# Kernel optimization log

Measured on AMD Instinct MI355X. Metric: run time of the kernel, lower is better.

Reference implementation:

```python
import jax, jax.numpy as jnp
import numpy as np

N_CAMS = 6
N_RAYS = 200
N_UNI = 32
N_G = 4
N_PG = 8
MAX_D = 100.0
SOM_SIG = 2.0
GRID_W = 400
RAW_W, RAW_H = 1600.0, 900.0
SCENE = np.array([-51.2, -51.2, -5.0, 51.2, 51.2, 3.0], dtype=np.float32)
LOSS_W = {'kl': 1.0, 'dist2closest': 0.01, 'color': 1.0, 'reprojection': 1.0}


def _pe(x):
    freqs = jnp.pi * (2.0 ** jnp.arange(6, dtype=x.dtype))
    xb = x[..., None, :] * freqs[:, None]
    flat = lambda t: t.reshape(t.shape[:-2] + (t.shape[-2] * t.shape[-1],))
    return jnp.concatenate([x, flat(jnp.sin(xb)), flat(jnp.cos(xb))], axis=-1)


def _bilinear(img, u, v):
    C, H, W = img.shape
    x0 = jnp.floor(u)
    y0 = jnp.floor(v)
    valid = (u >= 0) & (u <= W - 1) & (v >= 0) & (v <= H - 1)
    x0i = jnp.clip(x0.astype(jnp.int32), 0, W - 1)
    x1i = jnp.clip(x0i + 1, 0, W - 1)
    y0i = jnp.clip(y0.astype(jnp.int32), 0, H - 1)
    y1i = jnp.clip(y0i + 1, 0, H - 1)
    wx = u - x0
    wy = v - y0
    out = (img[:, y0i, x0i] * ((1 - wx) * (1 - wy))[None]
           + img[:, y0i, x1i] * (wx * (1 - wy))[None]
           + img[:, y1i, x0i] * ((1 - wx) * wy)[None]
           + img[:, y1i, x1i] * (wx * wy)[None])
    out = jnp.moveaxis(out, 0, -1) * valid[..., None]
    return out, valid


def _resnet_fc(feat, z, win, bin_, wz, bz, w0, b0, w1, b1, wout, bout):
    x = feat @ win + bin_
    for i in range(wz.shape[0]):
        x = x + z @ wz[i] + bz[i]
        h = jax.nn.relu(x)
        h = jax.nn.relu(h @ w0[i] + b0[i])
        h = h @ w1[i] + b1[i]
        x = x + h
    return jax.nn.relu(x) @ wout + bout


def _forward(cam_feat, bev_feat, source_imgs, target_imgs, raw_cam_Ks, source_cam_Ks,
             lidar2cams, source_cam2input_lidars, source_cam2target_cams,
             mlp_win, mlp_bin, mlp_wz, mlp_bz, mlp_w0, mlp_b0, mlp_w1, mlp_b1, mlp_wout, mlp_bout,
             g_win, g_bin, g_wz, g_bz, g_w0, g_b0, g_w1, g_b1, g_wout, g_bout, pixel_idx):
    cf = cam_feat[0]
    bf = bev_feat[0]
    si = source_imgs[0, 0]
    ti = target_imgs[0, 0]
    rK = raw_cam_Ks[0, :, :3, :3]
    sK = source_cam_Ks[0, 0, :, :3, :3]
    invK = jnp.linalg.inv(sK)
    l2c = lidar2cams[0]
    s2in = source_cam2input_lidars[0, 0]
    s2tg = source_cam2target_cams[0, 0]
    center = jnp.asarray((SCENE[:3] + SCENE[3:]) / 2.0)
    half = jnp.asarray((SCENE[3:] - SCENE[:3]) / 2.0)
    mlp_p = (mlp_win, mlp_bin, mlp_wz, mlp_bz, mlp_w0, mlp_b0, mlp_w1, mlp_b1, mlp_wout, mlp_bout)
    g_p = (g_win, g_bin, g_wz, g_bz, g_w0, g_b0, g_w1, g_b1, g_wout, g_bout)

    def per_cam(cf_c, si_c, ti_c, rK_c, sK_c, invK_c, l2c_c, s2in_c, s2tg_c, idx):
        N = idx.shape[0]
        x = (idx % GRID_W).astype(jnp.float32) * 2.0
        y = (idx // GRID_W).astype(jnp.float32) * 2.0
        pix_h = jnp.stack([x, y, jnp.ones_like(x)], axis=-1)
        dirs = pix_h @ invK_c.T
        d_u = (jnp.arange(N_UNI, dtype=jnp.float32) + 0.5) / N_UNI * MAX_D
        d_u_b = jnp.broadcast_to(d_u, (N, N_UNI))
        Hf, Wf = cf_c.shape[1], cf_c.shape[2]
        Hb, Wb = bf.shape[1], bf.shape[2]

        def eval_pts(d):
            pts_cam = dirs[:, None, :] * d[..., None]
            pts_lid = pts_cam @ s2in_c[:3, :3].T + s2in_c[:3, 3]
            pc = pts_lid @ l2c_c[:3, :3].T + l2c_c[:3, 3]
            z = pc[..., 2]
            zs = jnp.maximum(z, 1e-3)
            uvw = pc @ rK_c.T
            fu = uvw[..., 0] / zs * (Wf / RAW_W)
            fv = uvw[..., 1] / zs * (Hf / RAW_H)
            cam_lat, cval = _bilinear(cf_c, fu, fv)
            cval = cval & (z > 0.1)
            bx = (pts_lid[..., 0] - SCENE[0]) / (SCENE[3] - SCENE[0]) * (Wb - 1)
            by = (pts_lid[..., 1] - SCENE[1]) / (SCENE[4] - SCENE[1]) * (Hb - 1)
            bev_lat, bval = _bilinear(bf, bx, by)
            valid = cval & bval
            latent = jnp.concatenate([bev_lat, cam_lat], axis=-1) * valid[..., None]
            pln = (pts_lid - center) / half
            pcn = pts_cam / MAX_D
            vd = dirs / jnp.linalg.norm(dirs, axis=-1, keepdims=True)
            vdl = vd @ s2in_c[:3, :3].T
            vd_b = jnp.broadcast_to(vd[:, None, :], pcn.shape)
            vdl_b = jnp.broadcast_to(vdl[:, None, :], pcn.shape)
            feat = jnp.concatenate([_pe(pln), vdl_b, _pe(pcn), vd_b], axis=-1)
            return feat, latent, valid

        featc, latc, _valc = eval_pts(d_u_b)
        g = _resnet_fc(featc, latc, *g_p)
        logits = g[..., 0].reshape(N, N_G, N_PG)
        sval = g[..., 1].reshape(N, N_G, N_PG)
        wg = jax.nn.softmax(logits, axis=-1)
        d_grp = d_u.reshape(N_G, N_PG)
        mu = jnp.sum(wg * d_grp, axis=-1)
        std = jax.nn.softplus(jnp.sum(wg * sval, axis=-1)) + 0.1
        offs = jnp.linspace(-2.0, 2.0, N_PG)
        d_g = jnp.clip(mu[..., None] + std[..., None] * offs, 0.5, MAX_D).reshape(N, N_G * N_PG)
        d_all = jnp.sort(jnp.concatenate([d_u_b, d_g], axis=-1), axis=-1)

        featf, latf, valf = eval_pts(d_all)
        out = _resnet_fc(featf, latf, *mlp_p)
        rgb = jax.nn.sigmoid(out[..., :3])
        vf = valf.astype(jnp.float32)
        sigma = jax.nn.softplus(out[..., 3]) * vf
        delta = jnp.concatenate([d_all[..., 1:] - d_all[..., :-1],
                                 jnp.full((N, 1), 1e3, jnp.float32)], axis=-1)
        alpha = 1.0 - jnp.exp(-sigma * delta)
        trans = jnp.cumprod(1.0 - alpha + 1e-10, axis=-1)
        trans = jnp.concatenate([jnp.ones((N, 1), jnp.float32), trans[..., :-1]], axis=-1)
        w = alpha * trans
        color = jnp.sum(w[..., None] * rgb, axis=-2)
        depth = jnp.sum(w * d_all, axis=-1)
        rvr = vf.mean(axis=-1)

        dist2 = (d_all[:, None, :] - mu[:, :, None]) ** 2
        resp = jax.nn.softmax(-dist2 / (2.0 * SOM_SIG ** 2), axis=1)
        rw = resp * w[:, None, :] + 1e-8
        som_mean = jnp.sum(rw * d_all[:, None, :], axis=-1) / jnp.sum(rw, axis=-1)
        som_var = jnp.sum(rw * (d_all[:, None, :] - som_mean[..., None]) ** 2, axis=-1) / jnp.sum(rw, axis=-1)
        som_std = jnp.sqrt(som_var + 1e-6)
        kl = jnp.log(som_std / std) + (std ** 2 + (mu - som_mean) ** 2) / (2.0 * (som_var + 1e-6)) - 0.5
        loss_kl = kl.mean()

        dg = jnp.abs(mu - jax.lax.stop_gradient(depth)[:, None])
        loss_d2c = dg.min(axis=-1).mean()

        csrc, _ = _bilinear(si_c, x, y)
        loss_color = (jnp.abs(csrc - color) * rvr[:, None]).mean()

        pts_c = dirs * depth[:, None]
        pts_t = pts_c @ s2tg_c[:3, :3].T + s2tg_c[:3, 3]
        zt = jnp.maximum(pts_t[..., 2], 1e-3)
        uvt = pts_t @ sK_c.T
        pred, tval = _bilinear(ti_c, uvt[..., 0] / zt, uvt[..., 1] / zt)
        mask = (tval & (pts_t[..., 2] > 0.1) & (depth < 30.0)).astype(jnp.float32)
        l1 = jnp.abs(pred - csrc).mean(axis=-1)
        loss_re = jnp.sum(l1 * mask) / (jnp.sum(mask) + 1e-6)
        return loss_color, loss_kl, loss_d2c, loss_re

    lc, lkl, ld, lr = jax.vmap(per_cam)(cf, si, ti, rK, sK, invK, l2c, s2in, s2tg, pixel_idx)
    lr = jnp.where(jnp.isnan(lr), 0.0, lr)
    denom = float(N_CAMS)
    total = (LOSS_W['color'] * lc.sum() + LOSS_W['kl'] * lkl.sum()
             + LOSS_W['dist2closest'] * ld.sum() + LOSS_W['reprojection'] * lr.sum()) / denom
    return total


def setup_inputs() -> dict:
    key = jax.random.key(0)
    ks = jax.random.split(key, 8)
    f32 = jnp.float32
    cam_feat = jax.random.normal(ks[0], (1, 6, 256, 56, 100), f32)
    bev_feat = jax.random.normal(ks[1], (1, 512, 200, 200), f32)
    source_imgs = jax.random.uniform(ks[2], (1, 1, 6, 3, 300, 800), f32)
    target_imgs = jax.random.uniform(ks[3], (1, 1, 6, 3, 300, 800), f32)
    pixel_idx = jax.random.randint(ks[4], (6, N_RAYS), 0, GRID_W * 150)

    def rz(a):
        c, s = np.cos(a), np.sin(a)
        return np.array([[c, -s, 0.0], [s, c, 0.0], [0.0, 0.0, 1.0]], dtype=np.float32)
    A = np.array([[0, -1, 0], [0, 0, -1], [1, 0, 0]], dtype=np.float32)
    l2c = np.zeros((6, 4, 4), np.float32)
    for i in range(6):
        l2c[i, :3, :3] = A @ rz(-i * np.pi / 3)
        l2c[i, :3, 3] = np.array([0.0, 0.8, 0.5], np.float32)
        l2c[i, 3, 3] = 1.0
    s2in = np.linalg.inv(l2c).astype(np.float32)
    s2in[:, 0, 3] += 0.3
    s2tg = np.tile(np.eye(4, dtype=np.float32), (6, 1, 1))
    ang = 0.03
    s2tg[:, 0, 0] = np.cos(ang); s2tg[:, 0, 2] = np.sin(ang)
    s2tg[:, 2, 0] = -np.sin(ang); s2tg[:, 2, 2] = np.cos(ang)
    s2tg[:, 0, 3] = 0.3; s2tg[:, 2, 3] = 0.1
    rK = np.tile(np.eye(4, dtype=np.float32), (6, 1, 1))
    rK[:, 0, 0] = 800.0; rK[:, 1, 1] = 800.0; rK[:, 0, 2] = 800.0; rK[:, 1, 2] = 450.0
    sKm = np.tile(np.eye(4, dtype=np.float32), (6, 1, 1))
    sKm[:, 0, 0] = 400.0; sKm[:, 1, 1] = 400.0; sKm[:, 0, 2] = 400.0; sKm[:, 1, 2] = 150.0

    D_IN, D_H, D_LAT, NB = 84, 512, 768, 3

    def mk(k, dout):
        kk = jax.random.split(k, 5)
        return dict(
            win=jax.random.normal(kk[0], (D_IN, D_H), f32) * 0.1,
            bin=jnp.zeros((D_H,), f32),
            wz=jax.random.normal(kk[1], (NB, D_LAT, D_H), f32) * 0.036,
            bz=jnp.zeros((NB, D_H), f32),
            w0=jax.random.normal(kk[2], (NB, D_H, D_H), f32) * 0.044,
            b0=jnp.zeros((NB, D_H), f32),
            w1=jax.random.normal(kk[3], (NB, D_H, D_H), f32) * 0.044,
            b1=jnp.zeros((NB, D_H), f32),
            wout=jax.random.normal(kk[4], (D_H, dout), f32) * 0.044,
            bout=jnp.zeros((dout,), f32),
        )
    mp = mk(ks[5], 4)
    gp = mk(ks[6], 2)
    inp = {
        'cam_feat': cam_feat, 'bev_feat': bev_feat,
        'source_imgs': source_imgs, 'target_imgs': target_imgs,
        'raw_cam_Ks': jnp.asarray(rK)[None],
        'source_cam_Ks': jnp.asarray(sKm)[None, None],
        'lidar2cams': jnp.asarray(l2c)[None],
        'source_cam2input_lidars': jnp.asarray(s2in)[None, None],
        'source_cam2target_cams': jnp.asarray(s2tg)[None, None],
        'pixel_idx': pixel_idx,
    }
    for n, v in mp.items():
        inp['mlp_' + n] = v
    for n, v in gp.items():
        inp['g_' + n] = v
    return inp


def reference(cam_feat, bev_feat, source_imgs, target_imgs, raw_cam_Ks, source_cam_Ks,
              lidar2cams, source_cam2input_lidars, source_cam2target_cams,
              mlp_win, mlp_bin, mlp_wz, mlp_bz, mlp_w0, mlp_b0, mlp_w1, mlp_b1, mlp_wout, mlp_bout,
              g_win, g_bin, g_wz, g_bz, g_w0, g_b0, g_w1, g_b1, g_wout, g_bout, pixel_idx):
    return _forward(cam_feat, bev_feat, source_imgs, target_imgs, raw_cam_Ks, source_cam_Ks,
                    lidar2cams, source_cam2input_lidars, source_cam2target_cams,
                    mlp_win, mlp_bin, mlp_wz, mlp_bz, mlp_w0, mlp_b0, mlp_w1, mlp_b1, mlp_wout, mlp_bout,
                    g_win, g_bin, g_wz, g_bz, g_w0, g_b0, g_w1, g_b1, g_wout, g_bout, pixel_idx)
```

## Files before the change

kernel.cpp:

```cpp
#include <hip/hip_runtime.h>
#include <math.h>

typedef unsigned int uint32;
typedef short bf16x8 __attribute__((ext_vector_type(8)));
typedef float f32x4 __attribute__((ext_vector_type(4)));
typedef uint32 u32x2 __attribute__((ext_vector_type(2)));

__device__ __forceinline__ float sigmoidf_(float x){ return 1.0f/(1.0f+expf(-x)); }
__device__ __forceinline__ float softplusf_(float x){ return x>20.0f ? x : log1pf(expf(x)); }
__device__ __forceinline__ int iclampi(int v,int lo,int hi){ return v<lo?lo:(v>hi?hi:v); }

__device__ __forceinline__ float bf2f(uint32 u){ return __uint_as_float(u<<16); }
__device__ __forceinline__ unsigned short f2bf(float f){
  uint32 x = __float_as_uint(f);
  uint32 r = (x + 0x7fffu + ((x>>16)&1u)) >> 16;
  return (unsigned short)r;
}

typedef __attribute__((address_space(1))) const unsigned int ga_u32;
typedef __attribute__((address_space(3))) unsigned int ls_u32;
__device__ __forceinline__ void gl_lds16(const unsigned short* g, unsigned short* l){
  __builtin_amdgcn_global_load_lds((ga_u32*)g, (ls_u32*)l, 16, 0, 0);
}

__device__ __forceinline__ float pe_elem(int s, float vx, float vy, float vz){
  const float F0 = 3.14159265358979f;
  if (s < 3) return s==0?vx:(s==1?vy:vz);
  s -= 3;
  bool isCos = false;
  if (s >= 18){ s -= 18; isCos = true; }
  int fi = s/3, ci = s%3;
  float v = ci==0?vx:(ci==1?vy:vz);
  float f = F0 * (float)(1<<fi);
  return isCos ? cosf(f*v) : sinf(f*v);
}

__global__ __launch_bounds__(256) void transpose_cb_k(const float* __restrict__ in,
    unsigned short* __restrict__ out, int C, int S, int Cout,
    size_t inStride, size_t outStride, int rowStride)
{
  __shared__ float tile[32][33];
  int b = blockIdx.z;
  int s0 = blockIdx.x*32, c0 = blockIdx.y*32;
  int tx = threadIdx.x & 31, ty = threadIdx.x >> 5;
  #pragma unroll
  for (int i=0;i<32;i+=8){
    int c = c0+ty+i, s = s0+tx;
    tile[ty+i][tx] = (c<C && s<S) ? in[(size_t)b*inStride + (size_t)c*S + s] : 0.0f;
  }
  __syncthreads();
  #pragma unroll
  for (int i=0;i<32;i+=8){
    int s = s0+ty+i, c = c0+tx;
    if (s<S && c<Cout) out[(size_t)b*outStride + (size_t)s*rowStride + c] = f2bf(tile[tx][ty+i]);
  }
}

__global__ __launch_bounds__(256) void wprep_k(
    const float* __restrict__ g_wz, const float* __restrict__ m_wz,
    const float* __restrict__ g_win, const float* __restrict__ m_win,
    const float* __restrict__ g_w0, const float* __restrict__ m_w0,
    const float* __restrict__ g_w1, const float* __restrict__ m_w1,
    unsigned short* gWmT, unsigned short* mWmT,
    unsigned short* gW0T, unsigned short* mW0T,
    unsigned short* gW1Wz, unsigned short* mW1Wz,
    unsigned short* gW1T2, unsigned short* mW1T2,
    const float* __restrict__ m_b1, const float* __restrict__ m_bz,
    const float* __restrict__ g_b1, const float* __restrict__ g_bz,
    const float* __restrict__ m_bin, const float* __restrict__ g_bin,
    float* __restrict__ CB)
{
  __shared__ float tile[32][33];
  int l = blockIdx.x;
  const float* src; unsigned short* dst;
  int C, Cout, rs, s_t, c_t;
  if (l < 768){ int v=l/384, l2=l%384; s_t=l2%16; c_t=l2/16;
    src = v? m_wz : g_wz; dst = v? mWmT : gWmT; C=768; Cout=768; rs=896; }
  else if (l < 896){ int l0=l-768; int v=l0/64, l2=l0%64; s_t=l2%16; c_t=l2/16;
    src = v? m_win : g_win; dst = (v? mWmT : gWmT) + 768; C=84; Cout=128; rs=896; }
  else if (l < 2432){ int l0=l-896; int v=l0/768, l2=l0%768; int z=l2/256, l3=l2%256; s_t=l3%16; c_t=l3/16;
    src = (v? m_w0 : g_w0) + (size_t)z*512*512; dst = (v? mW0T : gW0T) + (size_t)z*512*512;
    C=512; Cout=512; rs=512; }
  else if (l < 3456){ int l0=l-2432; int v=l0/512, l2=l0%512; int z=l2/256, l3=l2%256; s_t=l3%16; c_t=l3/16;
    src = (v? m_w1 : g_w1) + (size_t)z*512*512; dst = (v? mW1Wz : gW1Wz) + (size_t)z*512*1280;
    C=512; Cout=512; rs=1280; }
  else if (l < 4992){ int l0=l-3456; int v=l0/768, l2=l0%768; int z=l2/384, l3=l2%384; s_t=l3%16; c_t=l3/16;
    src = (v? m_wz : g_wz) + (size_t)(z+1)*768*512; dst = (v? mW1Wz : gW1Wz) + 512 + (size_t)z*512*1280;
    C=768; Cout=768; rs=1280; }
  else if (l < 5504){ int l0=l-4992; int v=l0/256, l2=l0%256; s_t=l2%16; c_t=l2/16;
    src = (v? m_w1 : g_w1) + (size_t)2*512*512; dst = v? mW1T2 : gW1T2; C=512; Cout=512; rs=512; }
  else {
    int idx = (l-5504)*256 + threadIdx.x;
    if (idx < 3072){
      int w = idx >> 9, n = idx & 511;
      float v;
      if (w < 4){
        const float* b1 = (w < 2) ? m_b1 : g_b1;
        const float* bz = (w < 2) ? m_bz : g_bz;
        int i = w & 1;
        v = b1[i*512 + n] + bz[(i+1)*512 + n];
      } else if (w == 4) v = m_bin[n] + m_bz[n];
      else               v = g_bin[n] + g_bz[n];
      CB[idx] = v;
    }
    return;
  }
  int s0 = s_t*32, c0 = c_t*32;
  int tx = threadIdx.x & 31, ty = threadIdx.x >> 5;
  #pragma unroll
  for (int i=0;i<32;i+=8){
    int c = c0+ty+i, s = s0+tx;
    tile[ty+i][tx] = (c<C) ? src[(size_t)c*512 + s] : 0.0f;
  }
  __syncthreads();
  #pragma unroll
  for (int i=0;i<32;i+=8){
    int s = s0+ty+i, c = c0+tx;
    if (c<Cout) dst[(size_t)s*rs + c] = f2bf(tile[tx][ty+i]);
  }
}

__global__ void setup_rays_k(const int* __restrict__ pix, const float* __restrict__ sK_all,
                             const float* __restrict__ s2in_all,
                             float* __restrict__ dirs, float* __restrict__ vd,
                             float* __restrict__ vdl, float* __restrict__ acc)
{
  int r = blockIdx.x*blockDim.x + threadIdx.x;
  if (r >= 1200){ int z = r - 1200; if (z < 64) acc[z] = 0.0f; return; }
  int cam = r / 200;
  const float* sK = sK_all + cam*16;
  const float* s2in = s2in_all + cam*16;
  float a=sK[0],b=sK[1],c=sK[2],d=sK[4],e=sK[5],f=sK[6],g=sK[8],h=sK[9],i=sK[10];
  float det = a*(e*i-f*h) - b*(d*i-f*g) + c*(d*h-e*g);
  float inv00=(e*i-f*h)/det, inv01=(c*h-b*i)/det, inv02=(b*f-c*e)/det;
  float inv10=(f*g-d*i)/det, inv11=(a*i-c*g)/det, inv12=(c*d-a*f)/det;
  float inv20=(d*h-e*g)/det, inv21=(b*g-a*h)/det, inv22=(a*e-b*d)/det;
  int idx = pix[r];
  float x = (float)(idx % 400) * 2.0f;
  float y = (float)(idx / 400) * 2.0f;
  float dx = inv00*x + inv01*y + inv02;
  float dy = inv10*x + inv11*y + inv12;
  float dz = inv20*x + inv21*y + inv22;
  dirs[r*3+0]=dx; dirs[r*3+1]=dy; dirs[r*3+2]=dz;
  float n = sqrtf(dx*dx+dy*dy+dz*dz);
  float vx=dx/n, vy=dy/n, vz=dz/n;
  vd[r*3+0]=vx; vd[r*3+1]=vy; vd[r*3+2]=vz;
  vdl[r*3+0]=s2in[0]*vx + s2in[1]*vy + s2in[2]*vz;
  vdl[r*3+1]=s2in[4]*vx + s2in[5]*vy + s2in[6]*vz;
  vdl[r*3+2]=s2in[8]*vx + s2in[9]*vy + s2in[10]*vz;
}

__global__ __launch_bounds__(256) void eval2_k(
    const unsigned short* __restrict__ camT,
    const unsigned short* __restrict__ bevT,
    const float* __restrict__ dirs, const float* __restrict__ vd, const float* __restrict__ vdl,
    const float* __restrict__ dall, int ndepth, int R0, int P,
    const float* __restrict__ s2in_all, const float* __restrict__ l2c_all, const float* __restrict__ rK_all,
    unsigned short* __restrict__ cat, float* __restrict__ vf)
{
  int grp = threadIdx.x >> 7;
  int tl  = threadIdx.x & 127;
  int p = blockIdx.x*2 + grp;
  if (p >= P) return;
  int rl = p / ndepth;
  int j  = p - rl*ndepth;
  int R  = R0 + rl;
  int cam = R / 200;
  const float* s2in = s2in_all + cam*16;
  const float* l2c  = l2c_all + cam*16;
  const float* rK   = rK_all + cam*16;
  float dx = dirs[R*3+0], dy = dirs[R*3+1], dz = dirs[R*3+2];
  float d = dall ? dall[(size_t)rl*ndepth + j] : (((float)j + 0.5f)/32.0f)*100.0f;
  float px = dx*d, py = dy*d, pz = dz*d;
  float lx = s2in[0]*px + s2in[1]*py + s2in[2]*pz + s2in[3];
  float ly = s2in[4]*px + s2in[5]*py + s2in[6]*pz + s2in[7];
  float lz = s2in[8]*px + s2in[9]*py + s2in[10]*pz + s2in[11];
  float ccx = l2c[0]*lx + l2c[1]*ly + l2c[2]*lz + l2c[3];
  float ccy = l2c[4]*lx + l2c[5]*ly + l2c[6]*lz + l2c[7];
  float ccz = l2c[8]*lx + l2c[9]*ly + l2c[10]*lz + l2c[11];
  float zs = fmaxf(ccz, 0.001f);
  float uu = rK[0]*ccx + rK[1]*ccy + rK[2]*ccz;
  float vv = rK[4]*ccx + rK[5]*ccy + rK[6]*ccz;
  float fu = uu/zs*(100.0f/1600.0f);
  float fv = vv/zs*(56.0f/900.0f);
  bool cvalid = (fu>=0.0f)&&(fu<=99.0f)&&(fv>=0.0f)&&(fv<=55.0f)&&(ccz>0.1f);
  float cfx0 = floorf(fu), cfy0 = floorf(fv);
  int cx0=iclampi((int)cfx0,0,99), cx1=iclampi(cx0+1,0,99);
  int cy0=iclampi((int)cfy0,0,55), cy1=iclampi(cy0+1,0,55);
  float cwx=fu-cfx0, cwy=fv-cfy0;
  float cw00=(1-cwx)*(1-cwy), cw01=cwx*(1-cwy), cw10=(1-cwx)*cwy, cw11=cwx*cwy;
  float bx = (lx+51.2f)/102.4f*199.0f;
  float by = (ly+51.2f)/102.4f*199.0f;
  bool bvalid = (bx>=0.0f)&&(bx<=199.0f)&&(by>=0.0f)&&(by<=199.0f);
  float bfx0=floorf(bx), bfy0=floorf(by);
  int bx0=iclampi((int)bfx0,0,199), bx1=iclampi(bx0+1,0,199);
  int by0=iclampi((int)bfy0,0,199), by1=iclampi(by0+1,0,199);
  float bwx=bx-bfx0, bwy=by-bfy0;
  float bw00=(1-bwx)*(1-bwy), bw01=bwx*(1-bwy), bw10=(1-bwx)*bwy, bw11=bwx*bwy;
  float vflag = (cvalid && bvalid) ? 1.0f : 0.0f;
  uint32* catrow = (uint32*)(cat + (size_t)p*1408);
  auto bil2 = [&](uint32 a, uint32 b, uint32 c, uint32 dd,
                  float w00,float w01,float w10,float w11)->uint32{
    float lo = w00*bf2f(a&0xffffu)+w01*bf2f(b&0xffffu)+w10*bf2f(c&0xffffu)+w11*bf2f(dd&0xffffu);
    float hi = w00*bf2f(a>>16)+w01*bf2f(b>>16)+w10*bf2f(c>>16)+w11*bf2f(dd>>16);
    lo *= vflag; hi *= vflag;
    return (uint32)f2bf(lo) | ((uint32)f2bf(hi)<<16);
  };
  {
    size_t sb00 = (size_t)(by0*200+bx0)*512, sb01 = (size_t)(by0*200+bx1)*512;
    size_t sb10 = (size_t)(by1*200+bx0)*512, sb11 = (size_t)(by1*200+bx1)*512;
    u32x2 u00 = ((const u32x2*)(bevT + sb00))[tl];
    u32x2 u01 = ((const u32x2*)(bevT + sb01))[tl];
    u32x2 u10 = ((const u32x2*)(bevT + sb10))[tl];
    u32x2 u11 = ((const u32x2*)(bevT + sb11))[tl];
    u32x2 res;
    res[0] = bil2(u00[0],u01[0],u10[0],u11[0], bw00,bw01,bw10,bw11);
    res[1] = bil2(u00[1],u01[1],u10[1],u11[1], bw00,bw01,bw10,bw11);
    ((u32x2*)catrow)[128 + tl] = res;
  }
  {
    const unsigned short* cfT = camT + (size_t)cam*5600*256;
    size_t sc00 = (size_t)(cy0*100+cx0)*256, sc01 = (size_t)(cy0*100+cx1)*256;
    size_t sc10 = (size_t)(cy1*100+cx0)*256, sc11 = (size_t)(cy1*100+cx1)*256;
    uint32 u00 = ((const uint32*)(cfT + sc00))[tl];
    uint32 u01 = ((const uint32*)(cfT + sc01))[tl];
    uint32 u10 = ((const uint32*)(cfT + sc10))[tl];
    uint32 u11 = ((const uint32*)(cfT + sc11))[tl];
    catrow[512 + tl] = bil2(u00,u01,u10,u11, cw00,cw01,cw10,cw11);
  }
  if (tl < 64){
    float plx = lx/51.2f, ply = ly/51.2f, plz = (lz+1.0f)/4.0f;
    float pcx = px/100.0f, pcy = py/100.0f, pcz = pz/100.0f;
    float vx=vd[R*3], vy=vd[R*3+1], vz=vd[R*3+2];
    float wx=vdl[R*3], wy=vdl[R*3+1], wz=vdl[R*3+2];
    auto featv = [&](int s)->float{
      if (s >= 84) return 0.0f;
      if (s < 39)  return pe_elem(s, plx, ply, plz);
      if (s < 42)  return (s==39)?wx:((s==40)?wy:wz);
      if (s < 81)  return pe_elem(s-42, pcx, pcy, pcz);
      return (s==81)?vx:((s==82)?vy:vz);
    };
    float v0 = featv(2*tl), v1 = featv(2*tl+1);
    catrow[640 + tl] = (uint32)f2bf(v0) | ((uint32)f2bf(v1)<<16);
  }
  if (vf && tl==0) vf[p] = vflag;
}

#define GBM 128
#define GBN 128
#define GBK 64
template<int ACC, int RELU_OUT, int WRITE_XR>
__global__ __launch_bounds__(256) void mgemm_k(
    const unsigned short* __restrict__ A, int lda,
    const unsigned short* __restrict__ BT,
    const float* __restrict__ bias,
    unsigned short* __restrict__ C, int ldc,
    unsigned short* __restrict__ XR,
    int M, int N, int K)
{
  __shared__ unsigned short As[2][GBM*GBK];
  __shared__ unsigned short Bs[2][GBN*GBK];
  int w = blockIdx.x;
  int xcd = w & 7, ii = w >> 3;
  int colp = ii & 3, rgrp = ii >> 2;
  int rowp = rgrp*8 + xcd;
  int row0 = rowp*GBM, col0 = colp*GBN;
  if (row0 >= M) return;
  int tid = threadIdx.x;
  int lane = tid & 63, wave = tid >> 6;
  int wm = wave >> 1, wn = wave & 1;
  int l15 = lane & 15, l4 = lane >> 4;
  int lrow = lane >> 3;
  int lch  = lane & 7;
  int chsw = (lch ^ lrow) * 8;
  const unsigned short* aptr = A  + (size_t)(row0 + wave*32 + lrow)*lda + chsw;
  const unsigned short* bptr = BT + (size_t)(col0 + wave*32 + lrow)*K   + chsw;
  int woff = (wave*32)*64;

  auto STAGE = [&](int buf, int kk){
    unsigned short* ab = (buf ? &As[1][0] : &As[0][0]) + woff;
    unsigned short* bb = (buf ? &Bs[1][0] : &Bs[0][0]) + woff;
    #pragma unroll
    for (int i=0;i<4;++i) gl_lds16(aptr + (size_t)i*8*lda + kk, ab + i*8*64);
    #pragma unroll
    for (int i=0;i<4;++i) gl_lds16(bptr + (size_t)i*8*K   + kk, bb + i*8*64);
  };

  f32x4 acc[4][4];
  #pragma unroll
  for (int mi=0;mi<4;++mi)
    #pragma unroll
    for (int nj=0;nj<4;++nj){ f32x4 z = {0.f,0.f,0.f,0.f}; acc[mi][nj] = z; }

  STAGE(0, 0);
  int nk = K / GBK;
  for (int t=0; t<nk; ++t){
    __syncthreads();
    if (t+1 < nk) STAGE((t+1)&1, (t+1)*GBK);
    const unsigned short* Ab = (t&1) ? &As[1][0] : &As[0][0];
    const unsigned short* Bb = (t&1) ? &Bs[1][0] : &Bs[0][0];
    #pragma unroll
    for (int ks=0; ks<2; ++ks){
      bf16x8 a[4], b[4];
      #pragma unroll
      for (int mi=0;mi<4;++mi){
        int row = wm*64 + mi*16 + l15;
        int sc = (ks*4 + l4) ^ (row&7);
        a[mi] = *(const bf16x8*)&Ab[row*64 + sc*8];
      }
      #pragma unroll
      for (int nj=0;nj<4;++nj){
        int colr = wn*64 + nj*16 + l15;
        int sc = (ks*4 + l4) ^ (colr&7);
        b[nj] = *(const bf16x8*)&Bb[colr*64 + sc*8];
      }
      #pragma unroll
      for (int mi=0;mi<4;++mi)
        #pragma unroll
        for (int nj=0;nj<4;++nj)
          acc[mi][nj] = __builtin_amdgcn_mfma_f32_16x16x32_bf16(a[mi], b[nj], acc[mi][nj], 0,0,0);
    }
  }
  #pragma unroll
  for (int mi=0;mi<4;++mi){
    int gr0 = row0 + wm*64 + mi*16 + l4*4;
    #pragma unroll
    for (int nj=0;nj<4;++nj){
      int gc = col0 + wn*64 + nj*16 + l15;
      if (gc >= N) continue;
      float bv = bias[gc];
      #pragma unroll
      for (int i=0;i<4;++i){
        int gr = gr0 + i;
        if (gr >= M) continue;
        float v = acc[mi][nj][i] + bv;
        if (ACC) v += bf2f((uint32)C[(size_t)gr*ldc + gc]);
        if (RELU_OUT) v = fmaxf(v, 0.0f);
        C[(size_t)gr*ldc + gc] = f2bf(v);
        if (WRITE_XR) XR[(size_t)gr*512 + gc] = f2bf(fmaxf(v, 0.0f));
      }
    }
  }
}

static inline int gemm_grid(int M){
  int nrow = (M + GBM - 1)/GBM;
  int nrowp = (nrow + 7) & ~7;
  return nrowp * 4;
}

__global__ __launch_bounds__(256) void outlayer_w_k(const unsigned short* __restrict__ X,
    const float* __restrict__ W, const float* __restrict__ b, float* __restrict__ O,
    int M, int dout)
{
  int wid = threadIdx.x >> 6, lane = threadIdx.x & 63;
  int row = blockIdx.x*4 + wid;
  if (row >= M) return;
  const unsigned short* xr = X + (size_t)row*512;
  float s[4] = {0,0,0,0};
  for (int k=lane; k<512; k+=64){
    float xv = fmaxf(bf2f((uint32)xr[k]), 0.0f);
    #pragma unroll
    for (int c=0;c<4;++c)
      if (c < dout) s[c] += xv * W[(size_t)k*dout + c];
  }
  #pragma unroll
  for (int c=0;c<4;++c)
    #pragma unroll
    for (int m=32;m;m>>=1) s[c] += __shfl_xor(s[c], m, 64);
  if (lane == 0)
    for (int c=0;c<dout;++c) O[(size_t)row*dout + c] = s[c] + b[c];
}

__global__ __launch_bounds__(256) void coarse_post_w_k(const float* __restrict__ OUTB,
    float* __restrict__ MU, float* __restrict__ STD, float* __restrict__ DALL,
    int R0, int rn)
{
  int wid = threadIdx.x >> 6, lane = threadIdx.x & 63;
  int rl = blockIdx.x*4 + wid;
  if (rl >= rn) return;
  int R = R0 + rl;
  float v = 0.0f, muv = 0.0f, sdv = 0.0f;
  if (lane < 32){
    float lg = OUTB[((size_t)rl*32 + lane)*2 + 0];
    float sv = OUTB[((size_t)rl*32 + lane)*2 + 1];
    float mx = lg;
    #pragma unroll
    for (int m=1;m<8;m<<=1) mx = fmaxf(mx, __shfl_xor(mx, m, 64));
    float e = expf(lg - mx);
    float se = e;
    #pragma unroll
    for (int m=1;m<8;m<<=1) se += __shfl_xor(se, m, 64);
    float du = ((float)lane + 0.5f)/32.0f*100.0f;
    float wgt = e/se;
    float mp = wgt*du, sp = wgt*sv;
    #pragma unroll
    for (int m=1;m<8;m<<=1){ mp += __shfl_xor(mp, m, 64); sp += __shfl_xor(sp, m, 64); }
    muv = mp; sdv = softplusf_(sp) + 0.1f;
    if ((lane & 7) == 0){
      MU[R*4 + (lane>>3)] = muv;
      STD[R*4 + (lane>>3)] = sdv;
    }
    v = du;
  }
  {
    int g = (lane - 32) >> 3;
    int src = (lane >= 32) ? g*8 : 0;
    float mub = __shfl(muv, src, 64);
    float sdb = __shfl(sdv, src, 64);
    if (lane >= 32){
      int pp = (lane - 32) & 7;
      float off = -2.0f + (4.0f/7.0f)*(float)pp;
      v = fminf(fmaxf(mub + sdb*off, 0.5f), 100.0f);
    }
  }
  int rank = 0;
  for (int i=0;i<64;++i){
    float vi = __shfl(v, i, 64);
    rank += (vi < v) || (vi == v && i < lane);
  }
  DALL[(size_t)rl*64 + rank] = v;
}

__device__ __forceinline__ void bilin_img(const float* __restrict__ img, int H, int W,
                                          float u, float v, float* out3, bool* valid)
{
  *valid = (u>=0.0f)&&(u<=(float)(W-1))&&(v>=0.0f)&&(v<=(float)(H-1));
  float fx0=floorf(u), fy0=floorf(v);
  int x0=iclampi((int)fx0,0,W-1), x1=iclampi(x0+1,0,W-1);
  int y0=iclampi((int)fy0,0,H-1), y1=iclampi(y0+1,0,H-1);
  float wx=u-fx0, wy=v-fy0;
  float w00=(1-wx)*(1-wy), w01=wx*(1-wy), w10=(1-wx)*wy, w11=wx*wy;
  for (int ch=0; ch<3; ++ch){
    const float* p = img + (size_t)ch*H*W;
    out3[ch] = w00*p[y0*W+x0] + w01*p[y0*W+x1] + w10*p[y1*W+x0] + w11*p[y1*W+x1];
  }
}

__global__ __launch_bounds__(256) void render_loss_w_k(
  const float* __restrict__ OUTB, const float* __restrict__ VF,
  const float* __restrict__ DALL, const float* __restrict__ MU, const float* __restrict__ STD,
  const float* __restrict__ dirs, const int* __restrict__ pix,
  const float* __restrict__ src_imgs, const float* __restrict__ tgt_imgs,
  const float* __restrict__ s2tg_all, const float* __restrict__ sK_all,
  float* __restrict__ acc, int R0, int rn)
{
  int wid = threadIdx.x >> 6, lane = threadIdx.x & 63;
  int rl = blockIdx.x*4 + wid;
  if (rl >= rn) return;
  int R = R0 + rl;
  int cam = R / 200;
  int j = lane;
  float dj = DALL[(size_t)rl*64 + j];
  float delta = (j<63) ? (DALL[(size_t)rl*64 + j + 1] - dj) : 1000.0f;
  f32x4 o = *(const f32x4*)(OUTB + ((size_t)rl*64 + j)*4);
  float vfp = VF[(size_t)rl*64 + j];
  float sg = softplusf_(o[3])*vfp;
  float alpha = 1.0f - expf(-sg*delta);
  float prod = 1.0f - alpha + 1e-10f;
  #pragma unroll
  for (int dstep=1; dstep<64; dstep<<=1){
    float v = __shfl_up(prod, dstep, 64);
    if (lane >= dstep) prod *= v;
  }
  float T = __shfl_up(prod, 1, 64);
  if (lane == 0) T = 1.0f;
  float w = alpha*T;
  float c0 = w*sigmoidf_(o[0]), c1 = w*sigmoidf_(o[1]), c2 = w*sigmoidf_(o[2]);
  float dsum = w*dj, vs = vfp;
  #pragma unroll
  for (int m=32;m;m>>=1){
    c0 += __shfl_xor(c0,m,64); c1 += __shfl_xor(c1,m,64); c2 += __shfl_xor(c2,m,64);
    dsum += __shfl_xor(dsum,m,64); vs += __shfl_xor(vs,m,64);
  }
  float depth = dsum, rvr = vs/64.0f;
  float mu[4], sd[4];
  #pragma unroll
  for (int g=0;g<4;++g){ mu[g]=MU[R*4+g]; sd[g]=STD[R*4+g]; }
  float e[4], mx=-1e30f;
  #pragma unroll
  for (int g=0;g<4;++g){ float dd=dj-mu[g]; e[g]=-dd*dd*0.125f; mx=fmaxf(mx,e[g]); }
  float se=0;
  #pragma unroll
  for (int g=0;g<4;++g){ e[g]=expf(e[g]-mx); se+=e[g]; }
  float rw[4];
  #pragma unroll
  for (int g=0;g<4;++g) rw[g] = e[g]/se*w + 1e-8f;
  float srw[4], srwd[4];
  #pragma unroll
  for (int g=0;g<4;++g){ srw[g]=rw[g]; srwd[g]=rw[g]*dj; }
  #pragma unroll
  for (int m=32;m;m>>=1){
    #pragma unroll
    for (int g=0;g<4;++g){ srw[g]+=__shfl_xor(srw[g],m,64); srwd[g]+=__shfl_xor(srwd[g],m,64); }
  }
  float smean[4];
  #pragma unroll
  for (int g=0;g<4;++g) smean[g]=srwd[g]/srw[g];
  float sv[4];
  #pragma unroll
  for (int g=0;g<4;++g){ float dd=dj-smean[g]; sv[g]=rw[g]*dd*dd; }
  #pragma unroll
  for (int m=32;m;m>>=1){
    #pragma unroll
    for (int g=0;g<4;++g) sv[g]+=__shfl_xor(sv[g],m,64);
  }
  if (lane != 0) return;
  float klsum=0;
  #pragma unroll
  for (int g=0;g<4;++g){
    float var = sv[g]/srw[g];
    float sstd = sqrtf(var + 1e-6f);
    float dm = mu[g]-smean[g];
    klsum += logf(sstd/sd[g]) + (sd[g]*sd[g] + dm*dm)/(2.0f*(var+1e-6f)) - 0.5f;
  }
  float mind=1e30f;
  #pragma unroll
  for (int g=0;g<4;++g) mind = fminf(mind, fabsf(mu[g]-depth));
  const float* si = src_imgs + (size_t)cam*3*300*800;
  const float* ti = tgt_imgs + (size_t)cam*3*300*800;
  const float* s2tg = s2tg_all + cam*16;
  const float* sK = sK_all + cam*16;
  int idx = pix[R];
  float x = (float)(idx % 400) * 2.0f;
  float y = (float)(idx / 400) * 2.0f;
  float csrc[3]; bool sval;
  bilin_img(si, 300, 800, x, y, csrc, &sval);
  if (!sval){ csrc[0]=0; csrc[1]=0; csrc[2]=0; }
  float csum = fabsf(csrc[0]-c0)+fabsf(csrc[1]-c1)+fabsf(csrc[2]-c2);
  float dx=dirs[R*3], dy=dirs[R*3+1], dz=dirs[R*3+2];
  float px=dx*depth, py=dy*depth, pz=dz*depth;
  float tx=s2tg[0]*px+s2tg[1]*py+s2tg[2]*pz+s2tg[3];
  float ty=s2tg[4]*px+s2tg[5]*py+s2tg[6]*pz+s2tg[7];
  float tz=s2tg[8]*px+s2tg[9]*py+s2tg[10]*pz+s2tg[11];
  float zt=fmaxf(tz,0.001f);
  float uu=(sK[0]*tx+sK[1]*ty+sK[2]*tz)/zt;
  float vv=(sK[4]*tx+sK[5]*ty+sK[6]*tz)/zt;
  float pred[3]; bool tval;
  bilin_img(ti, 300, 800, uu, vv, pred, &tval);
  float tvf = tval?1.0f:0.0f;
  pred[0]*=tvf; pred[1]*=tvf; pred[2]*=tvf;
  float mask = (tval && (tz>0.1f) && (depth<30.0f)) ? 1.0f : 0.0f;
  float l1 = (fabsf(pred[0]-csrc[0])+fabsf(pred[1]-csrc[1])+fabsf(pred[2]-csrc[2]))*(1.0f/3.0f);
  float* a = acc + cam*8;
  atomicAdd(&a[0], csum*rvr);
  atomicAdd(&a[1], klsum);
  atomicAdd(&a[2], mind);
  atomicAdd(&a[3], l1*mask);
  atomicAdd(&a[4], mask);
}

__global__ void finalize_k(const float* __restrict__ acc, float* __restrict__ out){
  if (threadIdx.x==0 && blockIdx.x==0){
    float tot = 0.0f;
    for (int c=0;c<6;++c){
      const float* a = acc + c*8;
      float lc  = a[0] / 600.0f;
      float lkl = a[1] / 800.0f;
      float ld  = a[2] / 200.0f;
      float lr  = a[3] / (a[4] + 1e-6f);
      if (lr != lr) lr = 0.0f;
      tot += lc + lkl + 0.01f*ld + lr;
    }
    out[0] = tot / 6.0f;
  }
}

static void run_mlp5(hipStream_t stream, int M,
   const unsigned short* WmT, const float* CBin,
   const unsigned short* W0T, const float* b0,
   const unsigned short* W1Wz, const float* CB,
   const unsigned short* W1T2, const float* b1,
   const float* wout, const float* bout, int dout,
   unsigned short* CAT, unsigned short* X, unsigned short* XR, float* OUTB)
{
  int g = gemm_grid(M);
  mgemm_k<0,0,1><<<g,256,0,stream>>>(CAT+512, 1408, WmT, CBin, X, 512, XR, M, 512, 896);
  for (int i=0;i<2;++i){
    mgemm_k<0,1,0><<<g,256,0,stream>>>(XR, 512, W0T + (size_t)i*512*512, b0 + i*512, CAT, 1408, nullptr, M, 512, 512);
    mgemm_k<1,0,1><<<g,256,0,stream>>>(CAT, 1408, W1Wz + (size_t)i*512*1280, CB + i*512, X, 512, XR, M, 512, 1280);
  }
  mgemm_k<0,1,0><<<g,256,0,stream>>>(XR, 512, W0T + (size_t)2*512*512, b0 + 2*512, CAT, 1408, nullptr, M, 512, 512);
  mgemm_k<1,0,0><<<g,256,0,stream>>>(CAT, 1408, W1T2, b1 + 2*512, X, 512, nullptr, M, 512, 512);
  outlayer_w_k<<<(M+3)/4, 256, 0, stream>>>(X, wout, bout, OUTB, M, dout);
}

extern "C" void kernel_launch(void* const* d_in, const int* in_sizes, int n_in,
                              void* d_out, int out_size, void* d_ws, size_t ws_size,
                              hipStream_t stream) {
  (void)in_sizes; (void)n_in; (void)out_size;
  const float* cam_feat = (const float*)d_in[0];
  const float* bev_feat = (const float*)d_in[1];
  const float* src_imgs = (const float*)d_in[2];
  const float* tgt_imgs = (const float*)d_in[3];
  const float* rK   = (const float*)d_in[4];
  const float* sK   = (const float*)d_in[5];
  const float* l2c  = (const float*)d_in[6];
  const float* s2in = (const float*)d_in[7];
  const float* s2tg = (const float*)d_in[8];
  const int*   pix  = (const int*)d_in[9];
  const float* mlp_win = (const float*)d_in[10];
  const float* mlp_bin = (const float*)d_in[11];
  const float* mlp_wz  = (const float*)d_in[12];
  const float* mlp_bz  = (const float*)d_in[13];
  const float* mlp_w0  = (const float*)d_in[14];
  const float* mlp_b0  = (const float*)d_in[15];
  const float* mlp_w1  = (const float*)d_in[16];
  const float* mlp_b1  = (const float*)d_in[17];
  const float* mlp_wout= (const float*)d_in[18];
  const float* mlp_bout= (const float*)d_in[19];
  const float* g_win = (const float*)d_in[20];
  const float* g_bin = (const float*)d_in[21];
  const float* g_wz  = (const float*)d_in[22];
  const float* g_bz  = (const float*)d_in[23];
  const float* g_w0  = (const float*)d_in[24];
  const float* g_b0  = (const float*)d_in[25];
  const float* g_w1  = (const float*)d_in[26];
  const float* g_b1  = (const float*)d_in[27];
  const float* g_wout= (const float*)d_in[28];
  const float* g_bout= (const float*)d_in[29];

  char* base = (char*)d_ws;
  size_t off = 0;
  auto alloc = [&](size_t bytes)->char*{
    char* p = base + off;
    off = (off + bytes + 255) & ~(size_t)255;
    return p;
  };
  float* ACC  = (float*)alloc(64*4);
  float* DIR  = (float*)alloc(3600*4);
  float* VD   = (float*)alloc(3600*4);
  float* VDL  = (float*)alloc(3600*4);
  float* MU   = (float*)alloc(4800*4);
  float* STD  = (float*)alloc(4800*4);
  float* CBm  = (float*)alloc(3072*4);
  unsigned short* bevT = (unsigned short*)alloc((size_t)40000*512*2);
  unsigned short* camT = (unsigned short*)alloc((size_t)6*5600*256*2);
  unsigned short* gWmT  = (unsigned short*)alloc((size_t)512*896*2);
  unsigned short* mWmT  = (unsigned short*)alloc((size_t)512*896*2);
  unsigned short* gW0T  = (unsigned short*)alloc((size_t)3*512*512*2);
  unsigned short* mW0T  = (unsigned short*)alloc((size_t)3*512*512*2);
  unsigned short* gW1Wz = (unsigned short*)alloc((size_t)2*512*1280*2);
  unsigned short* mW1Wz = (unsigned short*)alloc((size_t)2*512*1280*2);
  unsigned short* gW1T2 = (unsigned short*)alloc((size_t)512*512*2);
  unsigned short* mW1T2 = (unsigned short*)alloc((size_t)512*512*2);
  size_t fixed = off;
  const size_t perray = 256 + 180224 + 65536 + 65536 + 1024 + 256;
  const size_t SLACK = 512*1024;
  int Rc = 1200;
  {
    size_t need = fixed + (size_t)1200*perray + SLACK + 8192;
    if (need > ws_size){
      size_t avail = (ws_size > fixed + SLACK + 8192) ? (ws_size - fixed - SLACK - 8192) : perray;
      Rc = (int)(avail / perray);
      if (Rc < 4) Rc = 4;
      Rc &= ~3;
      if (Rc > 1200) Rc = 1200;
    }
  }
  float*          DALL = (float*)alloc((size_t)Rc*64*4);
  unsigned short* CAT  = (unsigned short*)alloc((size_t)Rc*64*1408*2);
  unsigned short* X    = (unsigned short*)alloc((size_t)Rc*64*512*2);
  unsigned short* XR   = (unsigned short*)alloc((size_t)Rc*64*512*2);
  float*          OUTB = (float*)alloc((size_t)Rc*64*4*4);
  float*          VF   = (float*)alloc((size_t)Rc*64*4);

  { dim3 g((40000+31)/32, (512+31)/32, 1);
    transpose_cb_k<<<g,256,0,stream>>>(bev_feat, bevT, 512, 40000, 512, 0, 0, 512); }
  { dim3 g((5600+31)/32, (256+31)/32, 6);
    transpose_cb_k<<<g,256,0,stream>>>(cam_feat, camT, 256, 5600, 256, (size_t)256*5600, (size_t)5600*256, 256); }
  wprep_k<<<5516,256,0,stream>>>(
      g_wz, mlp_wz, g_win, mlp_win, g_w0, mlp_w0, g_w1, mlp_w1,
      gWmT, mWmT, gW0T, mW0T, gW1Wz, mW1Wz, gW1T2, mW1T2,
      mlp_b1, mlp_bz, g_b1, g_bz, mlp_bin, g_bin, CBm);

  setup_rays_k<<<5,256,0,stream>>>(pix, sK, s2in, DIR, VD, VDL, ACC);

  for (int R0=0; R0<1200; R0+=Rc){
    int rn = (1200 - R0 < Rc) ? (1200 - R0) : Rc;
    int Pc = rn*32;
    eval2_k<<<(Pc+1)/2,256,0,stream>>>(camT, bevT, DIR, VD, VDL,
        nullptr, 32, R0, Pc, s2in, l2c, rK, CAT, nullptr);
    run_mlp5(stream, Pc, gWmT, CBm+2560, gW0T, g_b0, gW1Wz, CBm+1024,
             gW1T2, g_b1, g_wout, g_bout, 2, CAT, X, XR, OUTB);
    coarse_post_w_k<<<(rn+3)/4,256,0,stream>>>(OUTB, MU, STD, DALL, R0, rn);
    int Pf = rn*64;
    eval2_k<<<(Pf+1)/2,256,0,stream>>>(camT, bevT, DIR, VD, VDL,
        DALL, 64, R0, Pf, s2in, l2c, rK, CAT, VF);
    run_mlp5(stream, Pf, mWmT, CBm+2048, mW0T, mlp_b0, mW1Wz, CBm,
             mW1T2, mlp_b1, mlp_wout, mlp_bout, 4, CAT, X, XR, OUTB);
    render_loss_w_k<<<(rn+3)/4,256,0,stream>>>(OUTB, VF, DALL, MU, STD,
        DIR, pix, src_imgs, tgt_imgs, s2tg, sK, ACC, R0, rn);
  }
  finalize_k<<<1,1,0,stream>>>(ACC, (float*)d_out);
}
```

Measured before the change: 2.043 ms.

## Load GEMM B operand directly into registers instead of staging through LDS

The B tile of the MLP GEMM is no longer copied into shared memory. Each wave now loads its B fragments from global memory straight into double-buffered registers. The main loop is unrolled by two so the A LDS buffers and the B register sets alternate explicitly. This halves LDS use and cuts LDS traffic, but it adds register pressure and issues uncoalesced-ish global loads that are duplicated across the waves sharing a column. The loop also assumes an even number of K tiles, since it always stages t+1.

```diff
diff --git a/kernel.cpp b/kernel.cpp
--- a/kernel.cpp
+++ b/kernel.cpp
@@ -259,7 +259,6 @@
     int M, int N, int K)
 {
   __shared__ unsigned short As[2][GBM*GBK];
-  __shared__ unsigned short Bs[2][GBN*GBK];
   int w = blockIdx.x;
   int xcd = w & 7, ii = w >> 3;
   int colp = ii & 3, rgrp = ii >> 2;
@@ -274,17 +273,22 @@
   int lch  = lane & 7;
   int chsw = (lch ^ lrow) * 8;
   const unsigned short* aptr = A  + (size_t)(row0 + wave*32 + lrow)*lda + chsw;
-  const unsigned short* bptr = BT + (size_t)(col0 + wave*32 + lrow)*K   + chsw;
+  const unsigned short* bpl  = BT + (size_t)(col0 + wn*64 + l15)*K + l4*8;
   int woff = (wave*32)*64;
 
-  auto STAGE = [&](int buf, int kk){
-    unsigned short* ab = (buf ? &As[1][0] : &As[0][0]) + woff;
-    unsigned short* bb = (buf ? &Bs[1][0] : &Bs[0][0]) + woff;
+  auto STAGEA = [&](int buf, int kk){
+    unsigned short* ab = &As[buf][0] + woff;
     #pragma unroll
     for (int i=0;i<4;++i) gl_lds16(aptr + (size_t)i*8*lda + kk, ab + i*8*64);
-    #pragma unroll
-    for (int i=0;i<4;++i) gl_lds16(bptr + (size_t)i*8*K   + kk, bb + i*8*64);
   };
+  bf16x8 bA[8], bB[8];
+  auto LOADB = [&](bf16x8* br, int kk){
+    #pragma unroll
+    for (int nj=0;nj<4;++nj)
+      #pragma unroll
+      for (int ks=0;ks<2;++ks)
+        br[nj*2+ks] = *(const bf16x8*)(bpl + (size_t)nj*16*K + kk + ks*32);
+  };
 
   f32x4 acc[4][4];
   #pragma unroll
@@ -292,16 +296,10 @@
     #pragma unroll
     for (int nj=0;nj<4;++nj){ f32x4 z = {0.f,0.f,0.f,0.f}; acc[mi][nj] = z; }
 
-  STAGE(0, 0);
-  int nk = K / GBK;
-  for (int t=0; t<nk; ++t){
-    __syncthreads();
-    if (t+1 < nk) STAGE((t+1)&1, (t+1)*GBK);
-    const unsigned short* Ab = (t&1) ? &As[1][0] : &As[0][0];
-    const unsigned short* Bb = (t&1) ? &Bs[1][0] : &Bs[0][0];
+  auto COMPUTE = [&](const unsigned short* Ab, const bf16x8* br){
     #pragma unroll
     for (int ks=0; ks<2; ++ks){
-      bf16x8 a[4], b[4];
+      bf16x8 a[4];
       #pragma unroll
       for (int mi=0;mi<4;++mi){
         int row = wm*64 + mi*16 + l15;
@@ -309,17 +307,24 @@
         a[mi] = *(const bf16x8*)&Ab[row*64 + sc*8];
       }
       #pragma unroll
-      for (int nj=0;nj<4;++nj){
-        int colr = wn*64 + nj*16 + l15;
-        int sc = (ks*4 + l4) ^ (colr&7);
-        b[nj] = *(const bf16x8*)&Bb[colr*64 + sc*8];
-      }
-      #pragma unroll
       for (int mi=0;mi<4;++mi)
         #pragma unroll
         for (int nj=0;nj<4;++nj)
-          acc[mi][nj] = __builtin_amdgcn_mfma_f32_16x16x32_bf16(a[mi], b[nj], acc[mi][nj], 0,0,0);
+          acc[mi][nj] = __builtin_amdgcn_mfma_f32_16x16x32_bf16(a[mi], br[nj*2+ks], acc[mi][nj], 0,0,0);
     }
+  };
+
+  int nk = K / GBK;
+  STAGEA(0, 0);
+  LOADB(bA, 0);
+  for (int t=0; t<nk; t+=2){
+    __syncthreads();
+    STAGEA(1, (t+1)*GBK);
+    LOADB(bB, (t+1)*GBK);
+    COMPUTE(&As[0][0], bA);
+    __syncthreads();
+    if (t+2 < nk){ STAGEA(0, (t+2)*GBK); LOADB(bA, (t+2)*GBK); }
+    COMPUTE(&As[1][0], bB);
   }
   #pragma unroll
   for (int mi=0;mi<4;++mi){
```

Result: slower. 2.868 ms (+40.4%).
